# Performance work log

Measured on AMD Instinct MI355X. Metric: run time of the kernel, lower is better.

## Reference

```python
import jax, jax.numpy as jnp
import numpy as np

N_NODES = 262144      # 2048 graphs * 128 nodes each
NUM_GRAPHS = 2048
MAX_NODES = 128
HIDDEN = 256
OUT_CH = 12
N_EDGES = 2097152     # ~avg degree 8


def setup_inputs() -> dict:
    key = jax.random.key(0)
    k1, k2, k3, k4 = jax.random.split(key, 4)
    x = jax.random.normal(k1, (N_NODES, HIDDEN), dtype=jnp.float32)
    # xavier-ish projection weight for Linear(6*hidden -> 12)
    W = jax.random.normal(k2, (OUT_CH, 6 * HIDDEN), dtype=jnp.float32) * (1.0 / np.sqrt(6 * HIDDEN))
    b = jnp.zeros((OUT_CH,), dtype=jnp.float32)
    # uniform graphs: sorted batch ids, MAX_NODES nodes per graph
    batch = (jnp.arange(N_NODES, dtype=jnp.int32) // MAX_NODES).astype(jnp.int32)
    # edges sampled within graphs: pick graph, then two local node ids
    g = jax.random.randint(k3, (N_EDGES,), 0, NUM_GRAPHS, dtype=jnp.int32)
    loc = jax.random.randint(k4, (N_EDGES, 2), 0, MAX_NODES, dtype=jnp.int32)
    src = g * MAX_NODES + loc[:, 0]
    dst = g * MAX_NODES + loc[:, 1]
    edge_index = jnp.stack([src, dst], axis=0).astype(jnp.int32)
    return {"x": x, "W": W, "b": b, "batch": batch, "edge_index": edge_index,
            "num_graphs": NUM_GRAPHS, "max_nodes": MAX_NODES}


def reference(x, W, b, batch, edge_index, num_graphs, max_nodes):
    N, H = x.shape
    G, M = num_graphs, max_nodes
    # local index of each node within its graph (batch is sorted by graph)
    counts = jax.ops.segment_sum(jnp.ones((N,), dtype=jnp.int32), batch, num_segments=G)
    starts = jnp.cumsum(counts) - counts            # exclusive prefix sum => first node of each graph
    local = jnp.arange(N, dtype=jnp.int32) - starts[batch]
    # dense per-graph node features X [G, M, H]
    X = jnp.zeros((G, M, H), dtype=x.dtype).at[batch, local].set(x)
    # dense symmetric adjacency A [G, M, M] (assignment semantics, like the torch loop)
    gi = batch[edge_index[0]]
    li = local[edge_index[0]]
    lj = local[edge_index[1]]
    A = jnp.zeros((G, M, M), dtype=x.dtype)
    A = A.at[gi, li, lj].set(1.0)
    A = A.at[gi, lj, li].set(1.0)
    # 6-gram walk readouts
    walk = X
    vs = [walk.sum(axis=1)]                          # v1
    for _ in range(5):                               # v2..v6
        walk = jnp.einsum('gnm,gmh->gnh', A, walk) * X
        vs.append(walk.sum(axis=1))
    out = jnp.concatenate(vs, axis=-1)               # == stack(dim=1).reshape(G, 6*H)
    out = out @ W.T + b                              # n_gram_projection
    return out
```

## Files before the change

### kernel.cpp

```cpp
#include <hip/hip_runtime.h>
#include <stdint.h>

#define NGRAPH 2048
#define MNODES 128
#define HID 256
#define OUTC 12
#define NEDGE 2097152

typedef __attribute__((ext_vector_type(8))) short short8;
typedef __attribute__((ext_vector_type(4))) float v4f;

#define SLICE 64
#define SWT_STRIDE 136

__device__ __forceinline__ unsigned short f2bf(float f) {
    unsigned int u = __builtin_bit_cast(unsigned int, f);
    u += 0x7fffu + ((u >> 16) & 1u);
    return (unsigned short)(u >> 16);
}

__global__ void build_bytes(const int* __restrict__ ei, unsigned char* __restrict__ Ab) {
    int e = blockIdx.x * blockDim.x + threadIdx.x;
    if (e >= NEDGE) return;
    int sN = ei[e];
    int dN = ei[NEDGE + e];
    int g = sN >> 7;
    int li = sN & 127;
    int lj = dN & 127;
    unsigned char* base = Ab + (size_t)g * (MNODES * MNODES);
    base[li * 128 + lj] = 1;
    base[lj * 128 + li] = 1;
}

__global__ void build_bits(const int* __restrict__ ei, unsigned int* __restrict__ bits) {
    int e = blockIdx.x * blockDim.x + threadIdx.x;
    if (e >= NEDGE) return;
    int sN = ei[e];
    int dN = ei[NEDGE + e];
    int g = sN >> 7;
    int li = sN & 127;
    int lj = dN & 127;
    unsigned int* base = bits + (size_t)g * (MNODES * 4);
    atomicOr(&base[li * 4 + (lj >> 5)], 1u << (lj & 31));
    atomicOr(&base[lj * 4 + (li >> 5)], 1u << (li & 31));
}

__launch_bounds__(256, 3)
__global__ void walk2(const float* __restrict__ x,
                      const float* __restrict__ W,
                      const unsigned char* __restrict__ Abytes,
                      const unsigned int* __restrict__ Abits,
                      int use_bytes,
                      float* __restrict__ partial) {
    __shared__ unsigned short sWT[SLICE][SWT_STRIDE];
    __shared__ float sVs2[2][6][SLICE];

    const int bx = blockIdx.x;
    const int g = bx >> 2;
    const int s = bx & 3;
    const int tid = threadIdx.x;
    const int wave = tid >> 6;
    const int lane = tid & 63;
    const int lrow = lane & 15;
    const int quad = lane >> 4;
    const int rhalf = wave >> 1;
    const int r0 = rhalf * 64;
    const int c0 = (wave & 1) * 32;
    const int cg0 = s * SLICE + c0;

    short8 areg[4][4];
    if (use_bytes) {
        const unsigned char* Ag = Abytes + (size_t)g * (MNODES * MNODES);
#pragma unroll
        for (int rt = 0; rt < 4; rt++) {
            int row = r0 + rt * 16 + lrow;
#pragma unroll
            for (int ks = 0; ks < 4; ks++) {
                int k0 = ks * 32 + quad * 8;
                uint2 u = *(const uint2*)(Ag + row * 128 + k0);
                short8 a;
#pragma unroll
                for (int j = 0; j < 8; j++) {
                    unsigned int byte = ((j < 4 ? u.x >> (8 * j) : u.y >> (8 * (j - 4))) & 0xFFu);
                    a[j] = (short)(byte ? 0x3F80 : 0);
                }
                areg[rt][ks] = a;
            }
        }
    } else {
        const unsigned int* Bg = Abits + (size_t)g * (MNODES * 4);
#pragma unroll
        for (int rt = 0; rt < 4; rt++) {
            int row = r0 + rt * 16 + lrow;
#pragma unroll
            for (int ks = 0; ks < 4; ks++) {
                unsigned int w = Bg[row * 4 + ks] >> (quad * 8);
                short8 a;
#pragma unroll
                for (int j = 0; j < 8; j++)
                    a[j] = (short)(((w >> j) & 1u) ? 0x3F80 : 0);
                areg[rt][ks] = a;
            }
        }
    }

    float xf[4][2][4];
    const float* xg = x + (size_t)g * (MNODES * HID);
#pragma unroll
    for (int rt = 0; rt < 4; rt++)
#pragma unroll
        for (int ct = 0; ct < 2; ct++) {
            int col = cg0 + ct * 16 + lrow;
#pragma unroll
            for (int reg = 0; reg < 4; reg++) {
                int row = r0 + rt * 16 + quad * 4 + reg;
                xf[rt][ct][reg] = xg[row * HID + col];
            }
        }
#pragma unroll
    for (int ct = 0; ct < 2; ct++) {
        int lcol = c0 + ct * 16 + lrow;
        float cs = 0.0f;
#pragma unroll
        for (int rt = 0; rt < 4; rt++) {
            int nbase = r0 + rt * 16 + quad * 4;
            uint2 u;
            u.x = (unsigned)f2bf(xf[rt][ct][0]) | ((unsigned)f2bf(xf[rt][ct][1]) << 16);
            u.y = (unsigned)f2bf(xf[rt][ct][2]) | ((unsigned)f2bf(xf[rt][ct][3]) << 16);
            *(uint2*)&sWT[lcol][nbase] = u;
            cs += xf[rt][ct][0] + xf[rt][ct][1] + xf[rt][ct][2] + xf[rt][ct][3];
        }
        cs += __shfl_xor(cs, 16);
        cs += __shfl_xor(cs, 32);
        if (quad == 0) sVs2[rhalf][0][lcol] = cs;
    }
    __syncthreads();

    for (int it = 1; it <= 5; it++) {
        v4f acc[4][2];
#pragma unroll
        for (int rt = 0; rt < 4; rt++)
#pragma unroll
            for (int ct = 0; ct < 2; ct++) acc[rt][ct] = (v4f)(0.0f);
#pragma unroll
        for (int ks = 0; ks < 4; ks++) {
            int k0 = ks * 32 + quad * 8;
#pragma unroll
            for (int ct = 0; ct < 2; ct++) {
                short8 bf = *(const short8*)&sWT[c0 + ct * 16 + lrow][k0];
#pragma unroll
                for (int rt = 0; rt < 4; rt++)
                    acc[rt][ct] = __builtin_amdgcn_mfma_f32_16x16x32_bf16(areg[rt][ks], bf, acc[rt][ct], 0, 0, 0);
            }
        }
        __syncthreads();
#pragma unroll
        for (int ct = 0; ct < 2; ct++) {
            int lcol = c0 + ct * 16 + lrow;
            float cs = 0.0f;
#pragma unroll
            for (int rt = 0; rt < 4; rt++) {
                float nw0 = acc[rt][ct][0] * xf[rt][ct][0];
                float nw1 = acc[rt][ct][1] * xf[rt][ct][1];
                float nw2 = acc[rt][ct][2] * xf[rt][ct][2];
                float nw3 = acc[rt][ct][3] * xf[rt][ct][3];
                int nbase = r0 + rt * 16 + quad * 4;
                uint2 u;
                u.x = (unsigned)f2bf(nw0) | ((unsigned)f2bf(nw1) << 16);
                u.y = (unsigned)f2bf(nw2) | ((unsigned)f2bf(nw3) << 16);
                *(uint2*)&sWT[lcol][nbase] = u;
                cs += nw0 + nw1 + nw2 + nw3;
            }
            cs += __shfl_xor(cs, 16);
            cs += __shfl_xor(cs, 32);
            if (quad == 0) sVs2[rhalf][it][lcol] = cs;
        }
        __syncthreads();
    }

    if (wave == 0) {
        for (int c = 0; c < OUTC; c++) {
            float p = 0.0f;
            const float* wr = W + c * (6 * HID);
#pragma unroll
            for (int ii = 0; ii < 6; ii++) {
                int i = ii * 64 + lane;
                int k = i >> 6;
                int h = i & 63;
                float v = sVs2[0][k][h] + sVs2[1][k][h];
                p += v * wr[k * HID + s * SLICE + h];
            }
#pragma unroll
            for (int off = 32; off >= 1; off >>= 1) p += __shfl_down(p, off);
            if (lane == 0) partial[bx * OUTC + c] = p;
        }
    }
}

__global__ void combine(const float* __restrict__ partial, const float* __restrict__ bvec,
                        float* __restrict__ out) {
    int i = blockIdx.x * blockDim.x + threadIdx.x;
    if (i >= NGRAPH * OUTC) return;
    int c = i % OUTC;
    int g = i / OUTC;
    float p = bvec[c];
#pragma unroll
    for (int s = 0; s < 4; s++) p += partial[(g * 4 + s) * OUTC + c];
    out[i] = p;
}

extern "C" void kernel_launch(void* const* d_in, const int* in_sizes, int n_in,
                              void* d_out, int out_size, void* d_ws, size_t ws_size,
                              hipStream_t stream) {
    const float* x = (const float*)d_in[0];
    const float* W = (const float*)d_in[1];
    const float* b = (const float*)d_in[2];
    const int* ei = (const int*)d_in[4];
    float* out = (float*)d_out;

    const size_t ABYTES = (size_t)NGRAPH * MNODES * MNODES;
    const size_t PARTIAL = (size_t)NGRAPH * 4 * OUTC * sizeof(float);

    if (ws_size >= ABYTES + PARTIAL) {
        unsigned char* Ab = (unsigned char*)d_ws;
        float* partial = (float*)((char*)d_ws + ABYTES);
        hipMemsetAsync(Ab, 0, ABYTES, stream);
        build_bytes<<<NEDGE / 256, 256, 0, stream>>>(ei, Ab);
        walk2<<<NGRAPH * 4, 256, 0, stream>>>(x, W, Ab, nullptr, 1, partial);
        combine<<<(NGRAPH * OUTC + 255) / 256, 256, 0, stream>>>(partial, b, out);
    } else {
        unsigned int* bits = (unsigned int*)d_ws;
        float* partial = (float*)((char*)d_ws + (size_t)NGRAPH * MNODES * 4 * 4);
        hipMemsetAsync(bits, 0, (size_t)NGRAPH * MNODES * 4 * 4, stream);
        build_bits<<<NEDGE / 512, 512, 0, stream>>>(ei, bits);
        walk2<<<NGRAPH * 4, 256, 0, stream>>>(x, W, nullptr, bits, 0, partial);
        combine<<<(NGRAPH * OUTC + 255) / 256, 256, 0, stream>>>(partial, b, out);
    }
}
```

Baseline: 502.6 us.

## Double-buffer walk LDS tile, use packed bf16 convert, spread projection across waves

The walk tile in shared memory is double-buffered so each iteration reads one buffer and writes the other, which removes one of the two block barriers per walk step. The software round-to-nearest bf16 conversion is replaced with the hardware packed v_cvt_pk_bf16_f32 instruction. The final 12-output projection is split so each of the four waves computes three outputs instead of wave 0 doing all twelve, and the launch bound now asks for 4 blocks per CU. The second buffer doubles the tile's LDS use, and the tighter launch bound may force register spills given the large areg/xf/acc register arrays.

```diff
diff --git a/kernel.cpp b/kernel.cpp
--- a/kernel.cpp
+++ b/kernel.cpp
@@ -13,10 +13,10 @@
 #define SLICE 64
 #define SWT_STRIDE 136
 
-__device__ __forceinline__ unsigned short f2bf(float f) {
-    unsigned int u = __builtin_bit_cast(unsigned int, f);
-    u += 0x7fffu + ((u >> 16) & 1u);
-    return (unsigned short)(u >> 16);
+__device__ __forceinline__ unsigned int cvtpk_bf16(float lo, float hi) {
+    unsigned int r;
+    asm("v_cvt_pk_bf16_f32 %0, %1, %2" : "=v"(r) : "v"(lo), "v"(hi));
+    return r;
 }
 
 __global__ void build_bytes(const int* __restrict__ ei, unsigned char* __restrict__ Ab) {
@@ -45,14 +45,14 @@
     atomicOr(&base[lj * 4 + (li >> 5)], 1u << (li & 31));
 }
 
-__launch_bounds__(256, 3)
+__launch_bounds__(256, 4)
 __global__ void walk2(const float* __restrict__ x,
                       const float* __restrict__ W,
                       const unsigned char* __restrict__ Abytes,
                       const unsigned int* __restrict__ Abits,
                       int use_bytes,
                       float* __restrict__ partial) {
-    __shared__ unsigned short sWT[SLICE][SWT_STRIDE];
+    __shared__ unsigned short sWT[2][SLICE][SWT_STRIDE];
     __shared__ float sVs2[2][6][SLICE];
 
     const int bx = blockIdx.x;
@@ -125,9 +125,9 @@
         for (int rt = 0; rt < 4; rt++) {
             int nbase = r0 + rt * 16 + quad * 4;
             uint2 u;
-            u.x = (unsigned)f2bf(xf[rt][ct][0]) | ((unsigned)f2bf(xf[rt][ct][1]) << 16);
-            u.y = (unsigned)f2bf(xf[rt][ct][2]) | ((unsigned)f2bf(xf[rt][ct][3]) << 16);
-            *(uint2*)&sWT[lcol][nbase] = u;
+            u.x = cvtpk_bf16(xf[rt][ct][0], xf[rt][ct][1]);
+            u.y = cvtpk_bf16(xf[rt][ct][2], xf[rt][ct][3]);
+            *(uint2*)&sWT[0][lcol][nbase] = u;
             cs += xf[rt][ct][0] + xf[rt][ct][1] + xf[rt][ct][2] + xf[rt][ct][3];
         }
         cs += __shfl_xor(cs, 16);
@@ -137,6 +137,8 @@
     __syncthreads();
 
     for (int it = 1; it <= 5; it++) {
+        const int cur = (it - 1) & 1;
+        const int nxt = it & 1;
         v4f acc[4][2];
 #pragma unroll
         for (int rt = 0; rt < 4; rt++)
@@ -147,13 +149,12 @@
             int k0 = ks * 32 + quad * 8;
 #pragma unroll
             for (int ct = 0; ct < 2; ct++) {
-                short8 bf = *(const short8*)&sWT[c0 + ct * 16 + lrow][k0];
+                short8 bf = *(const short8*)&sWT[cur][c0 + ct * 16 + lrow][k0];
 #pragma unroll
                 for (int rt = 0; rt < 4; rt++)
                     acc[rt][ct] = __builtin_amdgcn_mfma_f32_16x16x32_bf16(areg[rt][ks], bf, acc[rt][ct], 0, 0, 0);
             }
         }
-        __syncthreads();
 #pragma unroll
         for (int ct = 0; ct < 2; ct++) {
             int lcol = c0 + ct * 16 + lrow;
@@ -166,9 +167,9 @@
                 float nw3 = acc[rt][ct][3] * xf[rt][ct][3];
                 int nbase = r0 + rt * 16 + quad * 4;
                 uint2 u;
-                u.x = (unsigned)f2bf(nw0) | ((unsigned)f2bf(nw1) << 16);
-                u.y = (unsigned)f2bf(nw2) | ((unsigned)f2bf(nw3) << 16);
-                *(uint2*)&sWT[lcol][nbase] = u;
+                u.x = cvtpk_bf16(nw0, nw1);
+                u.y = cvtpk_bf16(nw2, nw3);
+                *(uint2*)&sWT[nxt][lcol][nbase] = u;
                 cs += nw0 + nw1 + nw2 + nw3;
             }
             cs += __shfl_xor(cs, 16);
@@ -178,17 +179,17 @@
         __syncthreads();
     }
 
-    if (wave == 0) {
-        for (int c = 0; c < OUTC; c++) {
+    {
+        int cbase = wave * 3;
+#pragma unroll
+        for (int cc = 0; cc < 3; cc++) {
+            int c = cbase + cc;
+            const float* wr = W + c * (6 * HID) + s * SLICE;
             float p = 0.0f;
-            const float* wr = W + c * (6 * HID);
-#pragma unroll
-            for (int ii = 0; ii < 6; ii++) {
-                int i = ii * 64 + lane;
-                int k = i >> 6;
-                int h = i & 63;
-                float v = sVs2[0][k][h] + sVs2[1][k][h];
-                p += v * wr[k * HID + s * SLICE + h];
+#pragma unroll
+            for (int k = 0; k < 6; k++) {
+                float v = sVs2[0][k][lane] + sVs2[1][k][lane];
+                p += v * wr[k * HID + lane];
             }
 #pragma unroll
             for (int off = 32; off >= 1; off >>= 1) p += __shfl_down(p, off);
```

Measured after the change: 668.3 us. 33.0% more time.
